# Kernel tuning notes

Measured on AMD Instinct MI355X. Metric: run time of the kernel, lower is better.

## Reference

```python
import jax, jax.numpy as jnp
import numpy as np
import math

SR = 96000.0
FRAME = 2048          # FRAME_SIZE
NB = 16               # N_BIQUADS
B, F = 16, 128        # batch, n_frames
N = F * FRAME         # n_samples (divisible by FRAME)

GAIN_RANGE = (-24.0, 24.0)
BROADBAND = (-60.0, 0.0)
Q_RANGE = (0.5, 16.0)
HPF_R = (20.0, 500.0)
LPF_R = (5000.0, 20000.0)
SHELF_R = (50.0, 16000.0)
PEAK_R = (100.0, 15000.0)


def _denorm_freq(n, r):
    lo, hi = math.log(r[0]), math.log(r[1])
    return jnp.exp(lo + n * (hi - lo))


def _denorm_gain(n, r):
    return r[0] + n * (r[1] - r[0])


def _denorm_q(n):
    lo, hi = math.log(Q_RANGE[0]), math.log(Q_RANGE[1])
    return jnp.exp(lo + n * (hi - lo))


def _norm(b0, b1, b2, a0, a1, a2):
    return b0 / a0, b1 / a0, b2 / a0, a1 / a0, a2 / a0


def _hp(fc, Q):
    w0 = 2 * math.pi * fc / SR
    al = jnp.sin(w0) / (2 * Q)
    c = jnp.cos(w0)
    return _norm((1 + c) / 2, -(1 + c), (1 + c) / 2, 1 + al, -2 * c, 1 - al)


def _lp(fc, Q):
    w0 = 2 * math.pi * fc / SR
    al = jnp.sin(w0) / (2 * Q)
    c = jnp.cos(w0)
    return _norm((1 - c) / 2, 1 - c, (1 - c) / 2, 1 + al, -2 * c, 1 - al)


def _peak(fc, g_db, Q):
    A = jnp.power(10.0, g_db / 40.0)
    w0 = 2 * math.pi * fc / SR
    al = jnp.sin(w0) / (2 * Q)
    c = jnp.cos(w0)
    return _norm(1 + al * A, -2 * c, 1 - al * A, 1 + al / A, -2 * c, 1 - al / A)


def _lowshelf(fc, g_db, Q):
    A = jnp.power(10.0, g_db / 40.0)
    w0 = 2 * math.pi * fc / SR
    al = jnp.sin(w0) / (2 * Q)
    c = jnp.cos(w0)
    sA = jnp.sqrt(A)
    b0 = A * (A + 1 - (A - 1) * c + 2 * sA * al)
    b1 = 2 * A * (A - 1 - (A + 1) * c)
    b2 = A * (A + 1 - (A - 1) * c - 2 * sA * al)
    a0 = A + 1 + (A - 1) * c + 2 * sA * al
    a1 = -2 * (A - 1 + (A + 1) * c)
    a2 = A + 1 + (A - 1) * c - 2 * sA * al
    return _norm(b0, b1, b2, a0, a1, a2)


def _highshelf(fc, g_db, Q):
    A = jnp.power(10.0, g_db / 40.0)
    w0 = 2 * math.pi * fc / SR
    al = jnp.sin(w0) / (2 * Q)
    c = jnp.cos(w0)
    sA = jnp.sqrt(A)
    b0 = A * (A + 1 + (A - 1) * c + 2 * sA * al)
    b1 = -2 * A * (A - 1 + (A + 1) * c)
    b2 = A * (A + 1 + (A - 1) * c - 2 * sA * al)
    a0 = A + 1 - (A - 1) * c + 2 * sA * al
    a1 = 2 * (A - 1 - (A + 1) * c)
    a2 = A + 1 - (A - 1) * c - 2 * sA * al
    return _norm(b0, b1, b2, a0, a1, a2)


def _forward(audio, params):
    b, n = audio.shape
    f = n // FRAME
    fp = params.shape[2]
    # per-audio-frame parameter index: min(frame_idx, n_frames_params-1)
    idx = jnp.minimum(jnp.arange(f), fp - 1)
    p = params[:, :, idx]                       # (B, 50, F)
    bq = p[:, : NB * 3, :].reshape(b, NB, 3, f)  # (B, 16, 3, F)
    in_g = jnp.power(10.0, _denorm_gain(p[:, -2, :], BROADBAND) / 20.0)   # (B,F)
    out_g = jnp.power(10.0, _denorm_gain(p[:, -1, :], BROADBAND) / 20.0)  # (B,F)

    x = audio.reshape(b, f, FRAME) * in_g[:, :, None]

    # per-stage normalized coefficients, each (B, F)
    coefs = []
    for i in range(NB):
        fn, gn, qn = bq[:, i, 0], bq[:, i, 1], bq[:, i, 2]
        Q = _denorm_q(qn)
        if i == 0:                      # BIQUAD_HPF
            c = _hp(_denorm_freq(fn, HPF_R), Q)
        elif i == NB - 1:               # BIQUAD_LPF
            c = _lp(_denorm_freq(fn, LPF_R), Q)
        elif i == 1:                    # BIQUAD_LOW_SHELF
            c = _lowshelf(_denorm_freq(fn, SHELF_R), _denorm_gain(gn, GAIN_RANGE), Q)
        elif i == NB - 2:               # BIQUAD_HIGH_SHELF
            c = _highshelf(_denorm_freq(fn, SHELF_R), _denorm_gain(gn, GAIN_RANGE), Q)
        else:                           # peaking EQ
            c = _peak(_denorm_freq(fn, PEAK_R), _denorm_gain(gn, GAIN_RANGE), Q)
        coefs.append(jnp.stack(c))      # (5, B, F)
    C = jnp.stack(coefs).reshape(NB, 5, b * f)  # (16, 5, B*F)

    # each (batch, frame) lane filters independently with zero initial state
    xt = x.reshape(b * f, FRAME).T              # (T, B*F)

    def step(s, v):
        # s: (16, 2, B*F) DF2T states; v: (B*F,) cascade input
        new_s = []
        for i in range(NB):
            b0, b1, b2, a1, a2 = C[i, 0], C[i, 1], C[i, 2], C[i, 3], C[i, 4]
            y = b0 * v + s[i, 0]
            s1 = b1 * v - a1 * y + s[i, 1]
            s2 = b2 * v - a2 * y
            new_s.append(jnp.stack([s1, s2]))
            v = y
        return jnp.stack(new_s), v

    s0 = jnp.zeros((NB, 2, b * f), dtype=audio.dtype)
    _, ys = jax.lax.scan(step, s0, xt)          # (T, B*F)

    y = ys.T.reshape(b, f, FRAME) * out_g[:, :, None]
    return y.reshape(b, n)


def setup_inputs() -> dict:
    key = jax.random.key(0)
    k1, k2 = jax.random.split(key)
    audio = jax.random.normal(k1, (B, N), dtype=jnp.float32)
    params = jax.random.uniform(k2, (B, 50, F), dtype=jnp.float32)
    return {"audio": audio, "params": params}


def reference(audio, params):
    return _forward(audio, params)
```

## Files before the change

### kernel.cpp

```cpp
#include <hip/hip_runtime.h>
#include <math.h>

namespace {

constexpr int kNB    = 16;
constexpr int kFrame = 2048;
constexpr int kChunk = 32;
constexpr int kWPB   = 4;

__global__ __launch_bounds__(256)
void biquad_chain_kernel(const float* __restrict__ audio,
                         const float* __restrict__ params,
                         float* __restrict__ out)
{
    __shared__ float sC[kWPB][kNB][5];
    __shared__ float sLvl[kWPB][kNB][6][3];

    const int tid  = threadIdx.x;
    const int wv   = tid >> 6;
    const int lane = tid & 63;
    const int ch   = blockIdx.x * kWPB + wv;
    const int bb   = ch >> 7;
    const int ff   = ch & 127;

    const float* pb = params + (size_t)bb * (50 * 128) + ff;

    if (lane < kNB) {
        const int band = lane;
        const double fn = (double)pb[(band * 3 + 0) * 128];
        const double gn = (double)pb[(band * 3 + 1) * 128];
        const double qn = (double)pb[(band * 3 + 2) * 128];
        const double PI = 3.14159265358979323846;
        const double SR = 96000.0;
        const double LN10 = 2.302585092994046;
        const double Q  = exp(log(0.5) + qn * (log(16.0) - log(0.5)));
        double b0, b1, b2, a0, a1, a2;
        if (band == 0) {
            const double fc = exp(log(20.0) + fn * (log(500.0) - log(20.0)));
            const double w0 = 2.0 * PI * fc / SR;
            const double al = sin(w0) / (2.0 * Q);
            const double c  = cos(w0);
            b0 = (1.0 + c) * 0.5; b1 = -(1.0 + c); b2 = (1.0 + c) * 0.5;
            a0 = 1.0 + al; a1 = -2.0 * c; a2 = 1.0 - al;
        } else if (band == kNB - 1) {
            const double fc = exp(log(5000.0) + fn * (log(20000.0) - log(5000.0)));
            const double w0 = 2.0 * PI * fc / SR;
            const double al = sin(w0) / (2.0 * Q);
            const double c  = cos(w0);
            b0 = (1.0 - c) * 0.5; b1 = 1.0 - c; b2 = (1.0 - c) * 0.5;
            a0 = 1.0 + al; a1 = -2.0 * c; a2 = 1.0 - al;
        } else if (band == 1) {
            const double fc = exp(log(50.0) + fn * (log(16000.0) - log(50.0)));
            const double g  = -24.0 + gn * 48.0;
            const double A  = exp(g * (LN10 / 40.0));
            const double w0 = 2.0 * PI * fc / SR;
            const double al = sin(w0) / (2.0 * Q);
            const double c  = cos(w0);
            const double sA2al = 2.0 * sqrt(A) * al;
            b0 = A * ((A + 1.0) - (A - 1.0) * c + sA2al);
            b1 = 2.0 * A * ((A - 1.0) - (A + 1.0) * c);
            b2 = A * ((A + 1.0) - (A - 1.0) * c - sA2al);
            a0 = (A + 1.0) + (A - 1.0) * c + sA2al;
            a1 = -2.0 * ((A - 1.0) + (A + 1.0) * c);
            a2 = (A + 1.0) + (A - 1.0) * c - sA2al;
        } else if (band == kNB - 2) {
            const double fc = exp(log(50.0) + fn * (log(16000.0) - log(50.0)));
            const double g  = -24.0 + gn * 48.0;
            const double A  = exp(g * (LN10 / 40.0));
            const double w0 = 2.0 * PI * fc / SR;
            const double al = sin(w0) / (2.0 * Q);
            const double c  = cos(w0);
            const double sA2al = 2.0 * sqrt(A) * al;
            b0 = A * ((A + 1.0) + (A - 1.0) * c + sA2al);
            b1 = -2.0 * A * ((A - 1.0) + (A + 1.0) * c);
            b2 = A * ((A + 1.0) + (A - 1.0) * c - sA2al);
            a0 = (A + 1.0) - (A - 1.0) * c + sA2al;
            a1 = 2.0 * ((A - 1.0) - (A + 1.0) * c);
            a2 = (A + 1.0) - (A - 1.0) * c - sA2al;
        } else {
            const double fc = exp(log(100.0) + fn * (log(15000.0) - log(100.0)));
            const double g  = -24.0 + gn * 48.0;
            const double A  = exp(g * (LN10 / 40.0));
            const double w0 = 2.0 * PI * fc / SR;
            const double al = sin(w0) / (2.0 * Q);
            const double c  = cos(w0);
            b0 = 1.0 + al * A; b1 = -2.0 * c; b2 = 1.0 - al * A;
            a0 = 1.0 + al / A; a1 = -2.0 * c; a2 = 1.0 - al / A;
        }
        const double inv = 1.0 / a0;
        b0 *= inv; b1 *= inv; b2 *= inv; a1 *= inv; a2 *= inv;

        if (band == 0) {
            const double in_g = exp((-60.0 + (double)pb[48 * 128] * 60.0) * (LN10 / 20.0));
            b0 *= in_g; b1 *= in_g; b2 *= in_g;
        }
        if (band == kNB - 1) {
            const double out_g = exp((-60.0 + (double)pb[49 * 128] * 60.0) * (LN10 / 20.0));
            b0 *= out_g; b1 *= out_g; b2 *= out_g;
        }

        sC[wv][band][0] = (float)b0;
        sC[wv][band][1] = (float)b1;
        sC[wv][band][2] = (float)b2;
        sC[wv][band][3] = (float)(-a1);
        sC[wv][band][4] = (float)(-a2);

        double al = 1.0, be = 0.0;
        #pragma unroll
        for (int s = 0; s < 10; ++s) {
            const double aln = al * (2.0 * be - a1 * al);
            const double ben = be * be - a2 * (al * al);
            al = aln; be = ben;
            if (s >= 4) {
                const int lvl = s - 4;
                sLvl[wv][band][lvl][0] = (float)al;
                sLvl[wv][band][lvl][1] = (float)be;
                sLvl[wv][band][lvl][2] = (float)(-a2 * al);
            }
        }
    }
    __syncthreads();

    float x[kChunk];
    {
        const float4* ap = reinterpret_cast<const float4*>(audio + (size_t)ch * kFrame + lane * kChunk);
        #pragma unroll
        for (int k = 0; k < kChunk / 4; ++k) {
            const float4 v = ap[k];
            x[4 * k + 0] = v.x;
            x[4 * k + 1] = v.y;
            x[4 * k + 2] = v.z;
            x[4 * k + 3] = v.w;
        }
    }

    for (int band = 0; band < kNB; ++band) {
        const float b0  = sC[wv][band][0];
        const float b1  = sC[wv][band][1];
        const float b2  = sC[wv][band][2];
        const float na1 = sC[wv][band][3];
        const float na2 = sC[wv][band][4];

        float s1 = 0.f, s2 = 0.f;
        #pragma unroll
        for (int t = 0; t < kChunk; ++t) {
            const float xv = x[t];
            const float y  = fmaf(b0, xv, s1);
            const float tm = fmaf(b1, xv, s2);
            s2 = fmaf(na2, y, b2 * xv);
            s1 = fmaf(na1, y, tm);
            x[t] = y;
        }

        float v0, v1;
        {
            const float e0 = __shfl_up(s1, 1);
            const float e1 = __shfl_up(s2, 1);
            v0 = (lane == 0) ? 0.f : e0;
            v1 = (lane == 0) ? 0.f : e1;
        }
        #pragma unroll
        for (int j = 0; j < 6; ++j) {
            const int s = 1 << j;
            const float alpha = sLvl[wv][band][j][0];
            const float beta  = sLvl[wv][band][j][1];
            const float gamma = sLvl[wv][band][j][2];
            float t0 = __shfl_up(v0, (unsigned)s);
            float t1 = __shfl_up(v1, (unsigned)s);
            const bool ok = (lane >= s);
            t0 = ok ? t0 : 0.f;
            t1 = ok ? t1 : 0.f;
            const float w = fmaf(na1, t0, t1);
            v0 = fmaf(alpha, w,  fmaf(beta, t0, v0));
            v1 = fmaf(gamma, t0, fmaf(beta, t1, v1));
        }

        float w0 = v0, w1 = v1;
        #pragma unroll
        for (int t = 0; t < kChunk; ++t) {
            const float c = w0;
            x[t] += c;
            w0 = fmaf(na1, c, w1);
            w1 = na2 * c;
        }
    }

    {
        float4* op = reinterpret_cast<float4*>(out + (size_t)ch * kFrame + lane * kChunk);
        #pragma unroll
        for (int k = 0; k < kChunk / 4; ++k) {
            float4 v;
            v.x = x[4 * k + 0];
            v.y = x[4 * k + 1];
            v.z = x[4 * k + 2];
            v.w = x[4 * k + 3];
            op[k] = v;
        }
    }
}

}

extern "C" void kernel_launch(void* const* d_in, const int* in_sizes, int n_in,
                              void* d_out, int out_size, void* d_ws, size_t ws_size,
                              hipStream_t stream)
{
    (void)d_ws; (void)ws_size; (void)n_in; (void)in_sizes;
    const float* audio  = (const float*)d_in[0];
    const float* params = (const float*)d_in[1];
    float* outp = (float*)d_out;

    const int channels = out_size / kFrame;
    const int blocks   = (channels + kWPB - 1) / kWPB;

    hipLaunchKernelGGL(biquad_chain_kernel, dim3(blocks), dim3(256), 0, stream,
                       audio, params, outp);
}
```

Before: 32.73 us.

## Split per-lane chunk into four interleaved sub-chains to expose ILP

Each lane's 32-sample chunk is now filtered as four independent 8-sample sub-chains that are interleaved, which breaks the serial FMA dependency chain inside each band. Local partial states are combined with a two-level in-register scan using precomputed stride-8 and stride-16 transition coefficients, and the carry-in corrections are fanned back out to the sub-chains. The coefficient table grows to hold the two extra levels. The cost is extra FMAs, more registers, and more float rounding through the combination steps.

```diff
diff --git a/kernel.cpp b/kernel.cpp
--- a/kernel.cpp
+++ b/kernel.cpp
@@ -6,6 +6,7 @@
 constexpr int kNB    = 16;
 constexpr int kFrame = 2048;
 constexpr int kChunk = 32;
+constexpr int kSub   = 8;
 constexpr int kWPB   = 4;
 
 __global__ __launch_bounds__(256)
@@ -14,7 +15,7 @@
                          float* __restrict__ out)
 {
     __shared__ float sC[kWPB][kNB][5];
-    __shared__ float sLvl[kWPB][kNB][6][3];
+    __shared__ float sLvl[kWPB][kNB][8][3];
 
     const int tid  = threadIdx.x;
     const int wv   = tid >> 6;
@@ -111,8 +112,8 @@
             const double aln = al * (2.0 * be - a1 * al);
             const double ben = be * be - a2 * (al * al);
             al = aln; be = ben;
-            if (s >= 4) {
-                const int lvl = s - 4;
+            if (s >= 2) {
+                const int lvl = s - 2;
                 sLvl[wv][band][lvl][0] = (float)al;
                 sLvl[wv][band][lvl][1] = (float)be;
                 sLvl[wv][band][lvl][2] = (float)(-a2 * al);
@@ -140,31 +141,54 @@
         const float b2  = sC[wv][band][2];
         const float na1 = sC[wv][band][3];
         const float na2 = sC[wv][band][4];
-
-        float s1 = 0.f, s2 = 0.f;
-        #pragma unroll
-        for (int t = 0; t < kChunk; ++t) {
-            const float xv = x[t];
-            const float y  = fmaf(b0, xv, s1);
-            const float tm = fmaf(b1, xv, s2);
-            s2 = fmaf(na2, y, b2 * xv);
-            s1 = fmaf(na1, y, tm);
-            x[t] = y;
+        const float al8  = sLvl[wv][band][0][0];
+        const float be8  = sLvl[wv][band][0][1];
+        const float ga8  = sLvl[wv][band][0][2];
+        const float al16 = sLvl[wv][band][1][0];
+        const float be16 = sLvl[wv][band][1][1];
+        const float ga16 = sLvl[wv][band][1][2];
+
+        float s1[4] = {0.f, 0.f, 0.f, 0.f};
+        float s2[4] = {0.f, 0.f, 0.f, 0.f};
+        #pragma unroll
+        for (int t = 0; t < kSub; ++t) {
+            #pragma unroll
+            for (int q = 0; q < 4; ++q) {
+                const float xv = x[kSub * q + t];
+                const float y  = fmaf(b0, xv, s1[q]);
+                const float tm = fmaf(b1, xv, s2[q]);
+                s2[q] = fmaf(na2, y, b2 * xv);
+                s1[q] = fmaf(na1, y, tm);
+                x[kSub * q + t] = y;
+            }
+        }
+
+        float d01_0, d01_1, d23_0, d23_1, dt0, dt1;
+        {
+            const float w01 = fmaf(na1, s1[0], s2[0]);
+            d01_0 = fmaf(al8, w01, fmaf(be8, s1[0], s1[1]));
+            d01_1 = fmaf(ga8, s1[0], fmaf(be8, s2[0], s2[1]));
+            const float w23 = fmaf(na1, s1[2], s2[2]);
+            d23_0 = fmaf(al8, w23, fmaf(be8, s1[2], s1[3]));
+            d23_1 = fmaf(ga8, s1[2], fmaf(be8, s2[2], s2[3]));
+            const float wt = fmaf(na1, d01_0, d01_1);
+            dt0 = fmaf(al16, wt, fmaf(be16, d01_0, d23_0));
+            dt1 = fmaf(ga16, d01_0, fmaf(be16, d01_1, d23_1));
         }
 
         float v0, v1;
         {
-            const float e0 = __shfl_up(s1, 1);
-            const float e1 = __shfl_up(s2, 1);
+            const float e0 = __shfl_up(dt0, 1);
+            const float e1 = __shfl_up(dt1, 1);
             v0 = (lane == 0) ? 0.f : e0;
             v1 = (lane == 0) ? 0.f : e1;
         }
         #pragma unroll
         for (int j = 0; j < 6; ++j) {
             const int s = 1 << j;
-            const float alpha = sLvl[wv][band][j][0];
-            const float beta  = sLvl[wv][band][j][1];
-            const float gamma = sLvl[wv][band][j][2];
+            const float alpha = sLvl[wv][band][j + 2][0];
+            const float beta  = sLvl[wv][band][j + 2][1];
+            const float gamma = sLvl[wv][band][j + 2][2];
             float t0 = __shfl_up(v0, (unsigned)s);
             float t1 = __shfl_up(v1, (unsigned)s);
             const bool ok = (lane >= s);
@@ -175,13 +199,34 @@
             v1 = fmaf(gamma, t0, fmaf(beta, t1, v1));
         }
 
-        float w0 = v0, w1 = v1;
-        #pragma unroll
-        for (int t = 0; t < kChunk; ++t) {
-            const float c = w0;
-            x[t] += c;
-            w0 = fmaf(na1, c, w1);
-            w1 = na2 * c;
+        float u0_0 = v0, u0_1 = v1;
+        float u1_0, u1_1, u2_0, u2_1, u3_0, u3_1;
+        {
+            const float wa = fmaf(na1, u0_0, u0_1);
+            u1_0 = fmaf(al8, wa, fmaf(be8, u0_0, s1[0]));
+            u1_1 = fmaf(ga8, u0_0, fmaf(be8, u0_1, s2[0]));
+            const float wb = fmaf(na1, u0_0, u0_1);
+            u2_0 = fmaf(al16, wb, fmaf(be16, u0_0, d01_0));
+            u2_1 = fmaf(ga16, u0_0, fmaf(be16, u0_1, d01_1));
+            const float wc = fmaf(na1, u2_0, u2_1);
+            u3_0 = fmaf(al8, wc, fmaf(be8, u2_0, s1[2]));
+            u3_1 = fmaf(ga8, u2_0, fmaf(be8, u2_1, s2[2]));
+        }
+
+        float w0[4], w1[4];
+        w0[0] = u0_0; w1[0] = u0_1;
+        w0[1] = u1_0; w1[1] = u1_1;
+        w0[2] = u2_0; w1[2] = u2_1;
+        w0[3] = u3_0; w1[3] = u3_1;
+        #pragma unroll
+        for (int t = 0; t < kSub; ++t) {
+            #pragma unroll
+            for (int q = 0; q < 4; ++q) {
+                const float c = w0[q];
+                x[kSub * q + t] += c;
+                w0[q] = fmaf(na1, c, w1[q]);
+                w1[q] = na2 * c;
+            }
         }
     }
 
```

Result: slower. 33.71 us (+3.0%).

## Process biquads in pairs with coupled scan and precompute coefficients in separate kernel

Applied to the files above, without the earlier changes.

Coefficient and scan-level computation moves out of the main kernel into a separate coef_kernel that writes per-channel, per-pair tables to workspace. The main kernel then processes two cascaded biquads per pass, using a coupled 4-state cross-lane prefix scan with precomputed cross-terms, so the number of shuffle scan rounds is halved. This spreads the double-precision coefficient setup across all threads instead of 16 lanes per wave. In exchange it adds a second kernel launch, a workspace round trip, and more shuffles and FMAs per scan level.

```diff
diff --git a/kernel.cpp b/kernel.cpp
--- a/kernel.cpp
+++ b/kernel.cpp
@@ -3,36 +3,36 @@
 
 namespace {
 
-constexpr int kNB    = 16;
-constexpr int kFrame = 2048;
-constexpr int kChunk = 32;
-constexpr int kWPB   = 4;
+constexpr int kNB     = 16;
+constexpr int kFrame  = 2048;
+constexpr int kChunk  = 32;
+constexpr int kWPB    = 4;
+constexpr int kPairs  = 8;
+constexpr int kPS     = 96;
 
 __global__ __launch_bounds__(256)
-void biquad_chain_kernel(const float* __restrict__ audio,
-                         const float* __restrict__ params,
-                         float* __restrict__ out)
+void coef_kernel(const float* __restrict__ params, float* __restrict__ ws)
 {
-    __shared__ float sC[kWPB][kNB][5];
-    __shared__ float sLvl[kWPB][kNB][6][3];
-
-    const int tid  = threadIdx.x;
-    const int wv   = tid >> 6;
-    const int lane = tid & 63;
-    const int ch   = blockIdx.x * kWPB + wv;
-    const int bb   = ch >> 7;
-    const int ff   = ch & 127;
-
+    const int job = blockIdx.x * 256 + threadIdx.x;
+    if (job >= 2048 * kPairs) return;
+    const int p  = job & 7;
+    const int ch = job >> 3;
+    const int bb = ch >> 7;
+    const int ff = ch & 127;
     const float* pb = params + (size_t)bb * (50 * 128) + ff;
 
-    if (lane < kNB) {
-        const int band = lane;
+    const double PI   = 3.14159265358979323846;
+    const double SR   = 96000.0;
+    const double LN10 = 2.302585092994046;
+
+    double B0[2], B1[2], B2[2], Ac1[2], Ac2[2];
+
+    #pragma unroll
+    for (int h = 0; h < 2; ++h) {
+        const int band = 2 * p + h;
         const double fn = (double)pb[(band * 3 + 0) * 128];
         const double gn = (double)pb[(band * 3 + 1) * 128];
         const double qn = (double)pb[(band * 3 + 2) * 128];
-        const double PI = 3.14159265358979323846;
-        const double SR = 96000.0;
-        const double LN10 = 2.302585092994046;
         const double Q  = exp(log(0.5) + qn * (log(16.0) - log(0.5)));
         double b0, b1, b2, a0, a1, a2;
         if (band == 0) {
@@ -56,13 +56,13 @@
             const double w0 = 2.0 * PI * fc / SR;
             const double al = sin(w0) / (2.0 * Q);
             const double c  = cos(w0);
-            const double sA2al = 2.0 * sqrt(A) * al;
-            b0 = A * ((A + 1.0) - (A - 1.0) * c + sA2al);
+            const double s2 = 2.0 * sqrt(A) * al;
+            b0 = A * ((A + 1.0) - (A - 1.0) * c + s2);
             b1 = 2.0 * A * ((A - 1.0) - (A + 1.0) * c);
-            b2 = A * ((A + 1.0) - (A - 1.0) * c - sA2al);
-            a0 = (A + 1.0) + (A - 1.0) * c + sA2al;
+            b2 = A * ((A + 1.0) - (A - 1.0) * c - s2);
+            a0 = (A + 1.0) + (A - 1.0) * c + s2;
             a1 = -2.0 * ((A - 1.0) + (A + 1.0) * c);
-            a2 = (A + 1.0) + (A - 1.0) * c - sA2al;
+            a2 = (A + 1.0) + (A - 1.0) * c - s2;
         } else if (band == kNB - 2) {
             const double fc = exp(log(50.0) + fn * (log(16000.0) - log(50.0)));
             const double g  = -24.0 + gn * 48.0;
@@ -70,13 +70,13 @@
             const double w0 = 2.0 * PI * fc / SR;
             const double al = sin(w0) / (2.0 * Q);
             const double c  = cos(w0);
-            const double sA2al = 2.0 * sqrt(A) * al;
-            b0 = A * ((A + 1.0) + (A - 1.0) * c + sA2al);
+            const double s2 = 2.0 * sqrt(A) * al;
+            b0 = A * ((A + 1.0) + (A - 1.0) * c + s2);
             b1 = -2.0 * A * ((A - 1.0) + (A + 1.0) * c);
-            b2 = A * ((A + 1.0) + (A - 1.0) * c - sA2al);
-            a0 = (A + 1.0) - (A - 1.0) * c + sA2al;
+            b2 = A * ((A + 1.0) + (A - 1.0) * c - s2);
+            a0 = (A + 1.0) - (A - 1.0) * c + s2;
             a1 = 2.0 * ((A - 1.0) - (A + 1.0) * c);
-            a2 = (A + 1.0) - (A - 1.0) * c - sA2al;
+            a2 = (A + 1.0) - (A - 1.0) * c - s2;
         } else {
             const double fc = exp(log(100.0) + fn * (log(15000.0) - log(100.0)));
             const double g  = -24.0 + gn * 48.0;
@@ -89,7 +89,6 @@
         }
         const double inv = 1.0 / a0;
         b0 *= inv; b1 *= inv; b2 *= inv; a1 *= inv; a2 *= inv;
-
         if (band == 0) {
             const double in_g = exp((-60.0 + (double)pb[48 * 128] * 60.0) * (LN10 / 20.0));
             b0 *= in_g; b1 *= in_g; b2 *= in_g;
@@ -98,90 +97,138 @@
             const double out_g = exp((-60.0 + (double)pb[49 * 128] * 60.0) * (LN10 / 20.0));
             b0 *= out_g; b1 *= out_g; b2 *= out_g;
         }
-
-        sC[wv][band][0] = (float)b0;
-        sC[wv][band][1] = (float)b1;
-        sC[wv][band][2] = (float)b2;
-        sC[wv][band][3] = (float)(-a1);
-        sC[wv][band][4] = (float)(-a2);
-
-        double al = 1.0, be = 0.0;
-        #pragma unroll
-        for (int s = 0; s < 10; ++s) {
-            const double aln = al * (2.0 * be - a1 * al);
-            const double ben = be * be - a2 * (al * al);
-            al = aln; be = ben;
-            if (s >= 4) {
-                const int lvl = s - 4;
-                sLvl[wv][band][lvl][0] = (float)al;
-                sLvl[wv][band][lvl][1] = (float)be;
-                sLvl[wv][band][lvl][2] = (float)(-a2 * al);
-            }
-        }
+        B0[h] = b0; B1[h] = b1; B2[h] = b2; Ac1[h] = a1; Ac2[h] = a2;
+    }
+
+    const double g2_1 = B1[1] - Ac1[1] * B0[1];
+    const double g2_2 = B2[1] - Ac2[1] * B0[1];
+
+    float* W = ws + (size_t)job * kPS;
+    W[0] = (float)B0[0]; W[1] = (float)B1[0]; W[2] = (float)B2[0];
+    W[3] = (float)(-Ac1[0]); W[4] = (float)(-Ac2[0]);
+    W[5] = (float)B0[1]; W[6] = (float)B1[1]; W[7] = (float)B2[1];
+    W[8] = (float)(-Ac1[1]); W[9] = (float)(-Ac2[1]);
+    W[10] = (float)g2_1; W[11] = (float)g2_2;
+
+    const double a11 = Ac1[0], a21 = Ac2[0], a12 = Ac1[1], a22 = Ac2[1];
+    double al1 = 1.0, be1 = 0.0, al2 = 1.0, be2 = 0.0;
+    double S00 = g2_1, S01 = 0.0, S10 = g2_2, S11 = 0.0;
+    #pragma unroll
+    for (int i = 1; i <= 10; ++i) {
+        const double P00 = be1 - a11 * al1, P01 = al1, P10 = -a21 * al1, P11 = be1;
+        const double Q00 = be2 - a12 * al2, Q01 = al2, Q10 = -a22 * al2, Q11 = be2;
+        const double nS00 = Q00 * S00 + Q01 * S10 + S00 * P00 + S01 * P10;
+        const double nS01 = Q00 * S01 + Q01 * S11 + S00 * P01 + S01 * P11;
+        const double nS10 = Q10 * S00 + Q11 * S10 + S10 * P00 + S11 * P10;
+        const double nS11 = Q10 * S01 + Q11 * S11 + S10 * P01 + S11 * P11;
+        S00 = nS00; S01 = nS01; S10 = nS10; S11 = nS11;
+        const double nal1 = al1 * (2.0 * be1 - a11 * al1);
+        const double nbe1 = be1 * be1 - a21 * (al1 * al1);
+        const double nal2 = al2 * (2.0 * be2 - a12 * al2);
+        const double nbe2 = be2 * be2 - a22 * (al2 * al2);
+        al1 = nal1; be1 = nbe1; al2 = nal2; be2 = nbe2;
+        if (i >= 5) {
+            const int j = i - 5;
+            float* L = W + 12 + 12 * j;
+            L[0] = (float)al1; L[1] = (float)be1; L[2] = (float)(-a21 * al1);
+            L[3] = (float)al2; L[4] = (float)be2; L[5] = (float)(-a22 * al2);
+            L[6] = (float)S00; L[7] = (float)S01; L[8] = (float)S10; L[9] = (float)S11;
+            L[10] = 0.f; L[11] = 0.f;
+        }
+    }
+}
+
+__global__ __launch_bounds__(256)
+void biquad_main(const float* __restrict__ audio, const float* __restrict__ ws,
+                 float* __restrict__ out)
+{
+    __shared__ float sP[kWPB * kPairs * kPS];
+
+    const int tid  = threadIdx.x;
+    const int wv   = tid >> 6;
+    const int lane = tid & 63;
+    const int ch   = blockIdx.x * kWPB + wv;
+
+    {
+        const float4* src = reinterpret_cast<const float4*>(
+            ws + (size_t)blockIdx.x * kWPB * kPairs * kPS);
+        float4* dst = reinterpret_cast<float4*>(sP);
+        constexpr int n4 = kWPB * kPairs * kPS / 4;
+        #pragma unroll
+        for (int i = 0; i < n4 / 256; ++i) dst[tid + 256 * i] = src[tid + 256 * i];
     }
     __syncthreads();
+
+    const float* Pch = sP + wv * (kPairs * kPS);
 
     float x[kChunk];
     {
-        const float4* ap = reinterpret_cast<const float4*>(audio + (size_t)ch * kFrame + lane * kChunk);
+        const float4* ap = reinterpret_cast<const float4*>(
+            audio + (size_t)ch * kFrame + lane * kChunk);
         #pragma unroll
         for (int k = 0; k < kChunk / 4; ++k) {
             const float4 v = ap[k];
-            x[4 * k + 0] = v.x;
-            x[4 * k + 1] = v.y;
-            x[4 * k + 2] = v.z;
-            x[4 * k + 3] = v.w;
-        }
-    }
-
-    for (int band = 0; band < kNB; ++band) {
-        const float b0  = sC[wv][band][0];
-        const float b1  = sC[wv][band][1];
-        const float b2  = sC[wv][band][2];
-        const float na1 = sC[wv][band][3];
-        const float na2 = sC[wv][band][4];
-
-        float s1 = 0.f, s2 = 0.f;
+            x[4 * k + 0] = v.x; x[4 * k + 1] = v.y;
+            x[4 * k + 2] = v.z; x[4 * k + 3] = v.w;
+        }
+    }
+
+    for (int p = 0; p < kPairs; ++p) {
+        const float* C = Pch + p * kPS;
+        const float b01 = C[0], b11 = C[1], b21 = C[2], na11 = C[3], na21 = C[4];
+        const float b02 = C[5], b12 = C[6], b22 = C[7], na12 = C[8], na22 = C[9];
+        const float g21 = C[10], g22 = C[11];
+
+        float s11 = 0.f, s12 = 0.f, s21 = 0.f, s22 = 0.f;
         #pragma unroll
         for (int t = 0; t < kChunk; ++t) {
             const float xv = x[t];
-            const float y  = fmaf(b0, xv, s1);
-            const float tm = fmaf(b1, xv, s2);
-            s2 = fmaf(na2, y, b2 * xv);
-            s1 = fmaf(na1, y, tm);
-            x[t] = y;
-        }
-
-        float v0, v1;
-        {
-            const float e0 = __shfl_up(s1, 1);
-            const float e1 = __shfl_up(s2, 1);
-            v0 = (lane == 0) ? 0.f : e0;
-            v1 = (lane == 0) ? 0.f : e1;
-        }
+            const float y1 = fmaf(b01, xv, s11);
+            const float t1 = fmaf(b11, xv, s12);
+            s12 = fmaf(na21, y1, b21 * xv);
+            s11 = fmaf(na11, y1, t1);
+            const float y2 = fmaf(b02, y1, s21);
+            const float t2 = fmaf(b12, y1, s22);
+            s22 = fmaf(na22, y2, b22 * y1);
+            s21 = fmaf(na12, y2, t2);
+            x[t] = y2;
+        }
+
+        float v1 = __shfl_up(s11, 1), v2 = __shfl_up(s12, 1);
+        float v3 = __shfl_up(s21, 1), v4 = __shfl_up(s22, 1);
+        if (lane == 0) { v1 = 0.f; v2 = 0.f; v3 = 0.f; v4 = 0.f; }
+
         #pragma unroll
         for (int j = 0; j < 6; ++j) {
             const int s = 1 << j;
-            const float alpha = sLvl[wv][band][j][0];
-            const float beta  = sLvl[wv][band][j][1];
-            const float gamma = sLvl[wv][band][j][2];
-            float t0 = __shfl_up(v0, (unsigned)s);
+            const float la1 = C[12 + 12 * j + 0], lb1 = C[12 + 12 * j + 1], lg1 = C[12 + 12 * j + 2];
+            const float la2 = C[12 + 12 * j + 3], lb2 = C[12 + 12 * j + 4], lg2 = C[12 + 12 * j + 5];
+            const float S00 = C[12 + 12 * j + 6], S01 = C[12 + 12 * j + 7];
+            const float S10 = C[12 + 12 * j + 8], S11 = C[12 + 12 * j + 9];
             float t1 = __shfl_up(v1, (unsigned)s);
+            float t2 = __shfl_up(v2, (unsigned)s);
+            float t3 = __shfl_up(v3, (unsigned)s);
+            float t4 = __shfl_up(v4, (unsigned)s);
             const bool ok = (lane >= s);
-            t0 = ok ? t0 : 0.f;
-            t1 = ok ? t1 : 0.f;
-            const float w = fmaf(na1, t0, t1);
-            v0 = fmaf(alpha, w,  fmaf(beta, t0, v0));
-            v1 = fmaf(gamma, t0, fmaf(beta, t1, v1));
-        }
-
-        float w0 = v0, w1 = v1;
+            t1 = ok ? t1 : 0.f; t2 = ok ? t2 : 0.f;
+            t3 = ok ? t3 : 0.f; t4 = ok ? t4 : 0.f;
+            const float w1 = fmaf(na11, t1, t2);
+            v1 = fmaf(la1, w1, fmaf(lb1, t1, v1));
+            v2 = fmaf(lg1, t1, fmaf(lb1, t2, v2));
+            const float w2 = fmaf(na12, t3, t4);
+            v3 = fmaf(la2, w2, fmaf(lb2, t3, fmaf(S00, t1, fmaf(S01, t2, v3))));
+            v4 = fmaf(lg2, t3, fmaf(lb2, t4, fmaf(S10, t1, fmaf(S11, t2, v4))));
+        }
+
+        float w11 = v1, w12 = v2, w21 = v3, w22 = v4;
         #pragma unroll
         for (int t = 0; t < kChunk; ++t) {
-            const float c = w0;
-            x[t] += c;
-            w0 = fmaf(na1, c, w1);
-            w1 = na2 * c;
+            x[t] += fmaf(b02, w11, w21);
+            const float n11 = fmaf(na11, w11, w12);
+            const float n12 = na21 * w11;
+            const float n21 = fmaf(g21, w11, fmaf(na12, w21, w22));
+            const float n22 = fmaf(g22, w11, na22 * w21);
+            w11 = n11; w12 = n12; w21 = n21; w22 = n22;
         }
     }
 
@@ -190,10 +237,8 @@
         #pragma unroll
         for (int k = 0; k < kChunk / 4; ++k) {
             float4 v;
-            v.x = x[4 * k + 0];
-            v.y = x[4 * k + 1];
-            v.z = x[4 * k + 2];
-            v.w = x[4 * k + 3];
+            v.x = x[4 * k + 0]; v.y = x[4 * k + 1];
+            v.z = x[4 * k + 2]; v.w = x[4 * k + 3];
             op[k] = v;
         }
     }
@@ -205,14 +250,16 @@
                               void* d_out, int out_size, void* d_ws, size_t ws_size,
                               hipStream_t stream)
 {
-    (void)d_ws; (void)ws_size; (void)n_in; (void)in_sizes;
+    (void)in_sizes; (void)n_in; (void)ws_size;
     const float* audio  = (const float*)d_in[0];
     const float* params = (const float*)d_in[1];
     float* outp = (float*)d_out;
+    float* ws   = (float*)d_ws;
 
     const int channels = out_size / kFrame;
-    const int blocks   = (channels + kWPB - 1) / kWPB;
-
-    hipLaunchKernelGGL(biquad_chain_kernel, dim3(blocks), dim3(256), 0, stream,
-                       audio, params, outp);
-}
+    const int jobs     = channels * kPairs;
+    hipLaunchKernelGGL(coef_kernel, dim3(jobs / 256), dim3(256), 0, stream,
+                       params, ws);
+    hipLaunchKernelGGL(biquad_main, dim3(channels / kWPB), dim3(256), 0, stream,
+                       audio, ws, outp);
+}
```

Result: slower. 42.72 us (+30.5%).

## Split per-lane chunk into two packed-FP32 half-chunks with extra scan level

Applied to the files above, without the earlier changes.

Each lane's 32-sample chunk is split into two 16-sample halves that are filtered together with packed v_pk_fma_f32 instructions, cutting the length of the serial recurrence per band in half. The two halves are joined by an extra 16-step propagation level before the wavefront shuffle scan, and the correction pass also uses packed ops. The coefficient setup is rewritten as branch-merged common code with the gain folded into the normalisation. This adds inline asm and slightly more scan bookkeeping, and the launch now assumes the channel count divides evenly by the block size.

```diff
diff --git a/kernel.cpp b/kernel.cpp
--- a/kernel.cpp
+++ b/kernel.cpp
@@ -5,8 +5,26 @@
 
 constexpr int kNB    = 16;
 constexpr int kFrame = 2048;
-constexpr int kChunk = 32;
+constexpr int kHalf  = 16;
 constexpr int kWPB   = 4;
+
+typedef float f32x2 __attribute__((ext_vector_type(2)));
+
+__device__ inline f32x2 pk_fma(f32x2 a, f32x2 b, f32x2 c) {
+    f32x2 d;
+    asm("v_pk_fma_f32 %0, %1, %2, %3" : "=v"(d) : "v"(a), "v"(b), "v"(c));
+    return d;
+}
+__device__ inline f32x2 pk_mul(f32x2 a, f32x2 b) {
+    f32x2 d;
+    asm("v_pk_mul_f32 %0, %1, %2" : "=v"(d) : "v"(a), "v"(b));
+    return d;
+}
+__device__ inline f32x2 pk_add(f32x2 a, f32x2 b) {
+    f32x2 d;
+    asm("v_pk_add_f32 %0, %1, %2" : "=v"(d) : "v"(a), "v"(b));
+    return d;
+}
 
 __global__ __launch_bounds__(256)
 void biquad_chain_kernel(const float* __restrict__ audio,
@@ -14,7 +32,7 @@
                          float* __restrict__ out)
 {
     __shared__ float sC[kWPB][kNB][5];
-    __shared__ float sLvl[kWPB][kNB][6][3];
+    __shared__ float sLvl[kWPB][kNB][7][3];
 
     const int tid  = threadIdx.x;
     const int wv   = tid >> 6;
@@ -30,74 +48,64 @@
         const double fn = (double)pb[(band * 3 + 0) * 128];
         const double gn = (double)pb[(band * 3 + 1) * 128];
         const double qn = (double)pb[(band * 3 + 2) * 128];
-        const double PI = 3.14159265358979323846;
-        const double SR = 96000.0;
+        const double PI   = 3.14159265358979323846;
         const double LN10 = 2.302585092994046;
-        const double Q  = exp(log(0.5) + qn * (log(16.0) - log(0.5)));
+
+        const bool isHP = (band == 0), isLP = (band == kNB - 1);
+        const bool isShelf = (band == 1) || (band == kNB - 2);
+        const double flo = isHP ? 2.995732273553991
+                        : isLP ? 8.517193191416238
+                        : isShelf ? 3.912023005428146
+                        : 4.605170185988092;
+        const double fsp = isHP ? 3.2188758248682006
+                        : isLP ? 1.3862943611198906
+                        : isShelf ? 5.768320995793772
+                        : 5.0106352940962555;
+
+        const double Q  = exp(-0.6931471805599453 + qn * 3.4657359027997265);
+        const double fc = exp(flo + fn * fsp);
+        const double w0 = (2.0 * PI / 96000.0) * fc;
+        const double sw = sin(w0);
+        const double cw = cos(w0);
+        const double al = sw / (2.0 * Q);
+        const double gdb = (isHP || isLP) ? 0.0 : (-24.0 + gn * 48.0);
+        const double A   = exp(gdb * (LN10 / 40.0));
+        const double sA  = sqrt(A);
+        const double ge = isHP ? (-60.0 + (double)pb[48 * 128] * 60.0) * (LN10 / 20.0)
+                        : isLP ? (-60.0 + (double)pb[49 * 128] * 60.0) * (LN10 / 20.0)
+                        : 0.0;
+        const double gm = exp(ge);
+
         double b0, b1, b2, a0, a1, a2;
-        if (band == 0) {
-            const double fc = exp(log(20.0) + fn * (log(500.0) - log(20.0)));
-            const double w0 = 2.0 * PI * fc / SR;
-            const double al = sin(w0) / (2.0 * Q);
-            const double c  = cos(w0);
-            b0 = (1.0 + c) * 0.5; b1 = -(1.0 + c); b2 = (1.0 + c) * 0.5;
-            a0 = 1.0 + al; a1 = -2.0 * c; a2 = 1.0 - al;
-        } else if (band == kNB - 1) {
-            const double fc = exp(log(5000.0) + fn * (log(20000.0) - log(5000.0)));
-            const double w0 = 2.0 * PI * fc / SR;
-            const double al = sin(w0) / (2.0 * Q);
-            const double c  = cos(w0);
-            b0 = (1.0 - c) * 0.5; b1 = 1.0 - c; b2 = (1.0 - c) * 0.5;
-            a0 = 1.0 + al; a1 = -2.0 * c; a2 = 1.0 - al;
+        if (isHP) {
+            b0 = (1.0 + cw) * 0.5; b1 = -(1.0 + cw); b2 = (1.0 + cw) * 0.5;
+            a0 = 1.0 + al; a1 = -2.0 * cw; a2 = 1.0 - al;
+        } else if (isLP) {
+            b0 = (1.0 - cw) * 0.5; b1 = 1.0 - cw; b2 = (1.0 - cw) * 0.5;
+            a0 = 1.0 + al; a1 = -2.0 * cw; a2 = 1.0 - al;
         } else if (band == 1) {
-            const double fc = exp(log(50.0) + fn * (log(16000.0) - log(50.0)));
-            const double g  = -24.0 + gn * 48.0;
-            const double A  = exp(g * (LN10 / 40.0));
-            const double w0 = 2.0 * PI * fc / SR;
-            const double al = sin(w0) / (2.0 * Q);
-            const double c  = cos(w0);
-            const double sA2al = 2.0 * sqrt(A) * al;
-            b0 = A * ((A + 1.0) - (A - 1.0) * c + sA2al);
-            b1 = 2.0 * A * ((A - 1.0) - (A + 1.0) * c);
-            b2 = A * ((A + 1.0) - (A - 1.0) * c - sA2al);
-            a0 = (A + 1.0) + (A - 1.0) * c + sA2al;
-            a1 = -2.0 * ((A - 1.0) + (A + 1.0) * c);
-            a2 = (A + 1.0) + (A - 1.0) * c - sA2al;
+            const double s2 = 2.0 * sA * al;
+            b0 = A * ((A + 1.0) - (A - 1.0) * cw + s2);
+            b1 = 2.0 * A * ((A - 1.0) - (A + 1.0) * cw);
+            b2 = A * ((A + 1.0) - (A - 1.0) * cw - s2);
+            a0 = (A + 1.0) + (A - 1.0) * cw + s2;
+            a1 = -2.0 * ((A - 1.0) + (A + 1.0) * cw);
+            a2 = (A + 1.0) + (A - 1.0) * cw - s2;
         } else if (band == kNB - 2) {
-            const double fc = exp(log(50.0) + fn * (log(16000.0) - log(50.0)));
-            const double g  = -24.0 + gn * 48.0;
-            const double A  = exp(g * (LN10 / 40.0));
-            const double w0 = 2.0 * PI * fc / SR;
-            const double al = sin(w0) / (2.0 * Q);
-            const double c  = cos(w0);
-            const double sA2al = 2.0 * sqrt(A) * al;
-            b0 = A * ((A + 1.0) + (A - 1.0) * c + sA2al);
-            b1 = -2.0 * A * ((A - 1.0) + (A + 1.0) * c);
-            b2 = A * ((A + 1.0) + (A - 1.0) * c - sA2al);
-            a0 = (A + 1.0) - (A - 1.0) * c + sA2al;
-            a1 = 2.0 * ((A - 1.0) - (A + 1.0) * c);
-            a2 = (A + 1.0) - (A - 1.0) * c - sA2al;
+            const double s2 = 2.0 * sA * al;
+            b0 = A * ((A + 1.0) + (A - 1.0) * cw + s2);
+            b1 = -2.0 * A * ((A - 1.0) + (A + 1.0) * cw);
+            b2 = A * ((A + 1.0) + (A - 1.0) * cw - s2);
+            a0 = (A + 1.0) - (A - 1.0) * cw + s2;
+            a1 = 2.0 * ((A - 1.0) - (A + 1.0) * cw);
+            a2 = (A + 1.0) - (A - 1.0) * cw - s2;
         } else {
-            const double fc = exp(log(100.0) + fn * (log(15000.0) - log(100.0)));
-            const double g  = -24.0 + gn * 48.0;
-            const double A  = exp(g * (LN10 / 40.0));
-            const double w0 = 2.0 * PI * fc / SR;
-            const double al = sin(w0) / (2.0 * Q);
-            const double c  = cos(w0);
-            b0 = 1.0 + al * A; b1 = -2.0 * c; b2 = 1.0 - al * A;
-            a0 = 1.0 + al / A; a1 = -2.0 * c; a2 = 1.0 - al / A;
-        }
-        const double inv = 1.0 / a0;
-        b0 *= inv; b1 *= inv; b2 *= inv; a1 *= inv; a2 *= inv;
-
-        if (band == 0) {
-            const double in_g = exp((-60.0 + (double)pb[48 * 128] * 60.0) * (LN10 / 20.0));
-            b0 *= in_g; b1 *= in_g; b2 *= in_g;
-        }
-        if (band == kNB - 1) {
-            const double out_g = exp((-60.0 + (double)pb[49 * 128] * 60.0) * (LN10 / 20.0));
-            b0 *= out_g; b1 *= out_g; b2 *= out_g;
-        }
+            b0 = 1.0 + al * A; b1 = -2.0 * cw; b2 = 1.0 - al * A;
+            a0 = 1.0 + al / A; a1 = -2.0 * cw; a2 = 1.0 - al / A;
+        }
+        const double inv  = 1.0 / a0;
+        const double binv = inv * gm;
+        b0 *= binv; b1 *= binv; b2 *= binv; a1 *= inv; a2 *= inv;
 
         sC[wv][band][0] = (float)b0;
         sC[wv][band][1] = (float)b1;
@@ -105,32 +113,34 @@
         sC[wv][band][3] = (float)(-a1);
         sC[wv][band][4] = (float)(-a2);
 
-        double al = 1.0, be = 0.0;
+        double ap = 1.0, bp = 0.0;
         #pragma unroll
         for (int s = 0; s < 10; ++s) {
-            const double aln = al * (2.0 * be - a1 * al);
-            const double ben = be * be - a2 * (al * al);
-            al = aln; be = ben;
-            if (s >= 4) {
-                const int lvl = s - 4;
-                sLvl[wv][band][lvl][0] = (float)al;
-                sLvl[wv][band][lvl][1] = (float)be;
-                sLvl[wv][band][lvl][2] = (float)(-a2 * al);
+            const double an = ap * (2.0 * bp - a1 * ap);
+            const double bn = bp * bp - a2 * (ap * ap);
+            ap = an; bp = bn;
+            if (s >= 3) {
+                const int L = s - 3;
+                sLvl[wv][band][L][0] = (float)ap;
+                sLvl[wv][band][L][1] = (float)bp;
+                sLvl[wv][band][L][2] = (float)(-a2 * ap);
             }
         }
     }
     __syncthreads();
 
-    float x[kChunk];
+    f32x2 X[kHalf];
     {
-        const float4* ap = reinterpret_cast<const float4*>(audio + (size_t)ch * kFrame + lane * kChunk);
-        #pragma unroll
-        for (int k = 0; k < kChunk / 4; ++k) {
-            const float4 v = ap[k];
-            x[4 * k + 0] = v.x;
-            x[4 * k + 1] = v.y;
-            x[4 * k + 2] = v.z;
-            x[4 * k + 3] = v.w;
+        const float4* ap = reinterpret_cast<const float4*>(
+            audio + (size_t)ch * kFrame + lane * 32);
+        #pragma unroll
+        for (int k = 0; k < 4; ++k) {
+            const float4 va = ap[k];
+            const float4 vb = ap[k + 4];
+            X[4 * k + 0] = f32x2{va.x, vb.x};
+            X[4 * k + 1] = f32x2{va.y, vb.y};
+            X[4 * k + 2] = f32x2{va.z, vb.z};
+            X[4 * k + 3] = f32x2{va.w, vb.w};
         }
     }
 
@@ -140,31 +150,40 @@
         const float b2  = sC[wv][band][2];
         const float na1 = sC[wv][band][3];
         const float na2 = sC[wv][band][4];
-
-        float s1 = 0.f, s2 = 0.f;
-        #pragma unroll
-        for (int t = 0; t < kChunk; ++t) {
-            const float xv = x[t];
-            const float y  = fmaf(b0, xv, s1);
-            const float tm = fmaf(b1, xv, s2);
-            s2 = fmaf(na2, y, b2 * xv);
-            s1 = fmaf(na1, y, tm);
-            x[t] = y;
-        }
+        const f32x2 b0p  = {b0, b0},  b1p = {b1, b1}, b2p = {b2, b2};
+        const f32x2 na1p = {na1, na1}, na2p = {na2, na2};
+
+        f32x2 s1 = {0.f, 0.f}, s2 = {0.f, 0.f};
+        #pragma unroll
+        for (int t = 0; t < kHalf; ++t) {
+            const f32x2 xv = X[t];
+            const f32x2 y  = pk_fma(b0p, xv, s1);
+            const f32x2 tm = pk_fma(b1p, xv, s2);
+            s2 = pk_fma(na2p, y, pk_mul(b2p, xv));
+            s1 = pk_fma(na1p, y, tm);
+            X[t] = y;
+        }
+
+        const float al16 = sLvl[wv][band][0][0];
+        const float be16 = sLvl[wv][band][0][1];
+        const float ga16 = sLvl[wv][band][0][2];
+        const float wf = fmaf(na1, s1.x, s2.x);
+        const float d0 = fmaf(al16, wf, fmaf(be16, s1.x, s1.y));
+        const float d1 = fmaf(ga16, s1.x, fmaf(be16, s2.x, s2.y));
 
         float v0, v1;
         {
-            const float e0 = __shfl_up(s1, 1);
-            const float e1 = __shfl_up(s2, 1);
+            const float e0 = __shfl_up(d0, 1);
+            const float e1 = __shfl_up(d1, 1);
             v0 = (lane == 0) ? 0.f : e0;
             v1 = (lane == 0) ? 0.f : e1;
         }
         #pragma unroll
         for (int j = 0; j < 6; ++j) {
             const int s = 1 << j;
-            const float alpha = sLvl[wv][band][j][0];
-            const float beta  = sLvl[wv][band][j][1];
-            const float gamma = sLvl[wv][band][j][2];
+            const float alpha = sLvl[wv][band][j + 1][0];
+            const float beta  = sLvl[wv][band][j + 1][1];
+            const float gamma = sLvl[wv][band][j + 1][2];
             float t0 = __shfl_up(v0, (unsigned)s);
             float t1 = __shfl_up(v1, (unsigned)s);
             const bool ok = (lane >= s);
@@ -175,26 +194,26 @@
             v1 = fmaf(gamma, t0, fmaf(beta, t1, v1));
         }
 
-        float w0 = v0, w1 = v1;
-        #pragma unroll
-        for (int t = 0; t < kChunk; ++t) {
-            const float c = w0;
-            x[t] += c;
-            w0 = fmaf(na1, c, w1);
-            w1 = na2 * c;
+        const float wr  = fmaf(na1, v0, v1);
+        const float uB0 = fmaf(al16, wr, fmaf(be16, v0, s1.x));
+        const float uB1 = fmaf(ga16, v0, fmaf(be16, v1, s2.x));
+
+        f32x2 w0 = {v0, uB0}, w1 = {v1, uB1};
+        #pragma unroll
+        for (int t = 0; t < kHalf; ++t) {
+            const f32x2 c = w0;
+            X[t] = pk_add(X[t], c);
+            w0 = pk_fma(na1p, c, w1);
+            w1 = pk_mul(na2p, c);
         }
     }
 
     {
-        float4* op = reinterpret_cast<float4*>(out + (size_t)ch * kFrame + lane * kChunk);
-        #pragma unroll
-        for (int k = 0; k < kChunk / 4; ++k) {
-            float4 v;
-            v.x = x[4 * k + 0];
-            v.y = x[4 * k + 1];
-            v.z = x[4 * k + 2];
-            v.w = x[4 * k + 3];
-            op[k] = v;
+        float4* op = reinterpret_cast<float4*>(out + (size_t)ch * kFrame + lane * 32);
+        #pragma unroll
+        for (int k = 0; k < 4; ++k) {
+            op[k]     = float4{X[4 * k + 0].x, X[4 * k + 1].x, X[4 * k + 2].x, X[4 * k + 3].x};
+            op[k + 4] = float4{X[4 * k + 0].y, X[4 * k + 1].y, X[4 * k + 2].y, X[4 * k + 3].y};
         }
     }
 }
@@ -211,7 +230,7 @@
     float* outp = (float*)d_out;
 
     const int channels = out_size / kFrame;
-    const int blocks   = (channels + kWPB - 1) / kWPB;
+    const int blocks   = channels / kWPB;
 
     hipLaunchKernelGGL(biquad_chain_kernel, dim3(blocks), dim3(256), 0, stream,
                        audio, params, outp);
```

After: 30.01 us. 8.3% less time.
